# Optimization experiments

Measured on AMD Instinct MI355X. Metric: run time of the kernel, lower is better.

The kernel has to match this reference:

```python
import jax, jax.numpy as jnp
import numpy as np

B, V = 128, 128000
NEG_INF = float('-inf')


def _apply_top_k(logits, top_ks):
    vocab = logits.shape[-1]
    valid_k = jnp.where(top_ks > 0, jnp.minimum(top_ks, vocab), vocab)  # [B]
    order = jnp.argsort(-logits, axis=-1)                 # descending sort indices [B,V]
    sorted_logits = jnp.take_along_axis(logits, order, axis=-1)
    ranks = jnp.arange(vocab)[None, :]                    # [1,V]
    keep = ranks < valid_k[:, None]
    masked_sorted = jnp.where(keep, sorted_logits, NEG_INF)
    rows = jnp.arange(logits.shape[0])[:, None]
    return jnp.zeros_like(logits).at[rows, order].set(masked_sorted)


def _apply_top_p(logits, top_ps):
    order = jnp.argsort(-logits, axis=-1)
    sorted_logits = jnp.take_along_axis(logits, order, axis=-1)
    sorted_probs = jax.nn.softmax(sorted_logits, axis=-1)
    cum = jnp.cumsum(sorted_probs, axis=-1)
    keep = cum < top_ps[:, None]
    keep = keep.at[:, 0].set(True)                        # always keep the top token
    masked_sorted = jnp.where(keep, sorted_logits, NEG_INF)
    rows = jnp.arange(logits.shape[0])[:, None]
    return jnp.zeros_like(logits).at[rows, order].set(masked_sorted)


def setup_inputs() -> dict:
    key = jax.random.key(0)
    k1, k2, k3, k4, k5 = jax.random.split(key, 5)
    logits = jax.random.normal(k1, (B, V), dtype=jnp.float32) * 4.0
    temperatures = jax.random.uniform(k2, (B,), dtype=jnp.float32) + 0.5  # [0.5, 1.5)
    top_ks = jax.random.randint(k3, (B,), 0, 100, dtype=jnp.int64)        # 0 -> disabled
    top_ps = jax.random.uniform(k4, (B,), dtype=jnp.float32)
    # uniform noise; reference converts to Exp(1) via -log(u)
    exp_noise_u = jax.random.uniform(k5, (B, V), dtype=jnp.float32, minval=1e-12, maxval=1.0)
    return {"logits": logits, "temperatures": temperatures, "top_ks": top_ks,
            "top_ps": top_ps, "exp_noise_u": exp_noise_u}


def reference(logits, temperatures, top_ks, top_ps, exp_noise_u):
    x = logits.astype(jnp.float32) / temperatures[:, None]
    x = _apply_top_k(x, top_ks)
    x = _apply_top_p(x, top_ps)
    probs = jax.nn.softmax(x, axis=-1)
    q = jnp.clip(-jnp.log(exp_noise_u), 1e-10)            # Exp(1) samples, clamped like torch
    sample_tokens = jnp.argmax(probs / q, axis=-1)
    return sample_tokens
```

## Files before the change

### kernel.cpp

```cpp
#include <hip/hip_runtime.h>
#include <math.h>

#define SA 8
#define SM 64
#define NB 4096
#define TA 256
#define TAA 512
#define HS 256
#define TBB 1024
#define SCT 256
#define CH (NB / SCT)
#define CAPSEG 512
#define GTOT (SA * CAPSEG)
#define MAXM1 16
#define GB1 16384
#define SUBC 512
#define EQC 64
#define FXS 1099511627776.0f
#define FXI (1.0f / 1099511627776.0f)

typedef unsigned u32;
typedef unsigned long long u64;

struct State {
  float m, Z2;
  int mode, k, r, eqn;
  u32 vstar;
  int eq[EQC];
};

struct Aux1 {
  u32 pfx;
  int ca;
  float ea;
  float S;
  float target;
};

struct ScanSh {
  u32 axc[SCT]; float axe[SCT];
  u32 sufc[SCT]; float sufe[SCT];
  int cbin[SCT]; u32 cca[SCT]; float cea[SCT];
  int fbin[SCT]; u32 fca[SCT]; float fea[SCT];
};

__device__ __forceinline__ u32 f2key(float f) {
  u32 u = __float_as_uint(f);
  return u ^ ((u >> 31) ? 0xFFFFFFFFu : 0x80000000u);
}
__device__ __forceinline__ float key2f(u32 k) {
  u32 u = (k & 0x80000000u) ? (k ^ 0x80000000u) : ~k;
  return __uint_as_float(u);
}
__device__ __forceinline__ int is_mode0(int k, int V) {
  return (k >= 1 && k <= 256 && k < V);
}

__device__ void scan_level(const u32* cnt, const u64* e0, ScanSh* ax,
                           u32* sprefix, int* scnt_above, float* sexp_above,
                           float target, int tid) {
  if (tid < SCT) {
    u32 cc = 0; float ce = 0.f; const int base = tid * CH;
    for (int j = 0; j < CH; ++j) { cc += cnt[base + j]; ce += (float)e0[base + j] * FXI; }
    ax->axc[tid] = cc; ax->axe[tid] = ce;
  }
  __syncthreads();
  if (tid == 0) {
    u32 rc = 0; float re = 0.f;
    for (int c = SCT - 1; c >= 0; --c) {
      ax->sufc[c] = rc; ax->sufe[c] = re;
      rc += ax->axc[c]; re += ax->axe[c];
    }
  }
  __syncthreads();
  if (tid < SCT) {
    const int base = tid * CH;
    u32 rc = ax->sufc[tid]; float re = ax->sufe[tid];
    int best = -1; u32 bca = 0; float bea = 0.f;
    int fb = -1; u32 ffca = 0; float ffea = 0.f;
    for (int b = base + CH - 1; b >= base; --b) {
      u32 c = cnt[b]; float ebv = (float)e0[b] * FXI;
      bool cross = (c > 0) && ((re + ebv) >= target);
      if (cross && best < 0) { best = b; bca = rc; bea = re; }
      if (c > 0) { fb = b; ffca = rc; ffea = re; }
      rc += c; re += ebv;
    }
    ax->cbin[tid] = best; ax->cca[tid] = bca; ax->cea[tid] = bea;
    ax->fbin[tid] = fb; ax->fca[tid] = ffca; ax->fea[tid] = ffea;
  }
  __syncthreads();
  if (tid == 0) {
    int bsel = -1; u32 ca = 0; float ea = 0.f;
    for (int c = 0; c < SCT; ++c) {
      int b = ax->cbin[c];
      if (b > bsel) { bsel = b; ca = ax->cca[c]; ea = ax->cea[c]; }
    }
    if (bsel < 0) {
      for (int c = 0; c < SCT; ++c) {
        int b = ax->fbin[c];
        if (b >= 0 && (bsel < 0 || b < bsel)) { bsel = b; ca = ax->fca[c]; ea = ax->fea[c]; }
      }
    }
    if (bsel < 0) bsel = 0;
    *sprefix = (u32)bsel;
    *scnt_above = (int)ca;
    *sexp_above = ea;
  }
  __syncthreads();
}

__global__ __launch_bounds__(TAA) void kA(const float* __restrict__ logits,
                                          const float* __restrict__ temps,
                                          const int* __restrict__ topks,
                                          float* __restrict__ maxpart,
                                          u32* __restrict__ scnt,
                                          float* __restrict__ candv,
                                          int* __restrict__ candi,
                                          u32* __restrict__ nm1, int V) {
  const int row = blockIdx.x, seg = blockIdx.y, tid = threadIdx.x;
  __shared__ u32 cnt[NB];
  __shared__ float sm[TAA];
  __shared__ u32 cs[HS];
  __shared__ int bb[HS];
  __shared__ int lcnt;
  __shared__ u32 sT;
  if (row == 0 && seg == 0 && tid == 0) nm1[0] = 0;
  const int k = topks[row];
  const int m0 = is_mode0(k, V);
  const float t = temps[row];
  const float* lr = logits + (size_t)row * V;
  const float4* l4 = (const float4*)lr;
  const int n4 = V >> 2;
  const int q0 = (int)((long long)seg * n4 / SA);
  const int q1 = (int)((long long)(seg + 1) * n4 / SA);
  float mx = -INFINITY;
  if (m0) {
    for (int i = tid; i < NB; i += TAA) cnt[i] = 0;
    if (tid == 0) lcnt = 0;
    __syncthreads();
    for (int i = q0 + tid; i < q1; i += TAA) {
      float4 v = l4[i];
      float xs[4] = {v.x / t, v.y / t, v.z / t, v.w / t};
#pragma unroll
      for (int j = 0; j < 4; ++j) {
        mx = fmaxf(mx, xs[j]);
        atomicAdd(&cnt[f2key(xs[j]) >> 20], 1u);
      }
    }
    if (seg == SA - 1)
      for (int i = (n4 << 2) + tid; i < V; i += TAA) {
        float x = lr[i] / t;
        mx = fmaxf(mx, x);
        atomicAdd(&cnt[f2key(x) >> 20], 1u);
      }
  } else {
    for (int i = q0 + tid; i < q1; i += TAA) {
      float4 v = l4[i];
      mx = fmaxf(mx, fmaxf(fmaxf(v.x, v.y), fmaxf(v.z, v.w)) / t);
    }
    if (seg == SA - 1)
      for (int i = (n4 << 2) + tid; i < V; i += TAA) mx = fmaxf(mx, lr[i] / t);
  }
  sm[tid] = mx;
  __syncthreads();
  for (int s = TAA >> 1; s > 0; s >>= 1) {
    if (tid < s) sm[tid] = fmaxf(sm[tid], sm[tid + s]);
    __syncthreads();
  }
  if (tid == 0) maxpart[row * SA + seg] = sm[0];
  if (!m0) return;
  if (tid < HS) {
    u32 cc = 0; const int base = tid * (NB / HS);
    for (int j = 0; j < NB / HS; ++j) cc += cnt[base + j];
    cs[tid] = cc;
  }
  __syncthreads();
  if (tid == 0) {
    u32 rc = 0;
    for (int c = HS - 1; c >= 0; --c) { u32 tmp = cs[c]; cs[c] = rc; rc += tmp; }
  }
  __syncthreads();
  const int kk = (k > 256) ? 256 : k;
  if (tid < HS) {
    const int base = tid * (NB / HS);
    u32 rc = cs[tid]; int best = -1;
    for (int b = base + NB / HS - 1; b >= base; --b) {
      u32 c = cnt[b];
      if (c && best < 0 && (int)(rc + c) >= kk) best = b;
      rc += c;
    }
    bb[tid] = best;
  }
  __syncthreads();
  if (tid == 0) {
    int bsel = -1;
    for (int c = 0; c < HS; ++c) if (bb[c] > bsel) bsel = bb[c];
    if (bsel < 0) { for (int b = 0; b < NB; ++b) if (cnt[b]) { bsel = b; break; } }
    if (bsel < 0) bsel = 0;
    sT = ((u32)bsel) << 20;
  }
  __syncthreads();
  const u32 T = sT;
  const size_t cbase = ((size_t)row * SA + seg) * CAPSEG;
  for (int i = q0 + tid; i < q1; i += TAA) {
    float4 v = l4[i];
    float xs[4] = {v.x / t, v.y / t, v.z / t, v.w / t};
#pragma unroll
    for (int j = 0; j < 4; ++j) {
      if (f2key(xs[j]) >= T) {
        int s = atomicAdd(&lcnt, 1);
        if (s < CAPSEG) { candv[cbase + s] = xs[j]; candi[cbase + s] = i * 4 + j; }
      }
    }
  }
  if (seg == SA - 1)
    for (int i = (n4 << 2) + tid; i < V; i += TAA) {
      float x = lr[i] / t;
      if (f2key(x) >= T) {
        int s = atomicAdd(&lcnt, 1);
        if (s < CAPSEG) { candv[cbase + s] = x; candi[cbase + s] = i; }
      }
    }
  __syncthreads();
  if (tid == 0) { int n = lcnt; if (n > CAPSEG) n = CAPSEG; scnt[row * SA + seg] = (u32)n; }
}

__global__ __launch_bounds__(TBB) void kB(const int* __restrict__ topks,
                                          const float* __restrict__ maxpart,
                                          State* __restrict__ st,
                                          u64* __restrict__ rpack,
                                          u32* __restrict__ nm1,
                                          u32* __restrict__ m1rows,
                                          u32* __restrict__ zp, size_t zwords, int V) {
  const int row = blockIdx.x, tid = threadIdx.x;
  State* rs = &st[row];
  const int k = topks[row];
  const int m0 = is_mode0(k, V);
  if (tid == 0) {
    float m = maxpart[row * SA];
    for (int j = 1; j < SA; ++j) m = fmaxf(m, maxpart[row * SA + j]);
    rs->m = m; rs->mode = m0 ? 0 : 1; rs->k = k; rs->eqn = 0; rs->r = 0;
    if (!m0) {
      int idx = (int)atomicAdd(nm1, 1u);
      if (idx < MAXM1) m1rows[idx] = (u32)row;
      rpack[row] = 0ull;
    }
  }
  const size_t stride = (size_t)gridDim.x * blockDim.x;
  for (size_t i = (size_t)blockIdx.x * blockDim.x + tid; i < zwords; i += stride) zp[i] = 0;
}

__global__ __launch_bounds__(TA) void kC(const float* __restrict__ logits,
                                         const float* __restrict__ temps,
                                         const State* __restrict__ st,
                                         const u32* __restrict__ nm1,
                                         const u32* __restrict__ m1rows,
                                         float* __restrict__ Sparts,
                                         u32* __restrict__ m1c0,
                                         u64* __restrict__ m1e0, int V) {
  u32 n = nm1[0]; if (n > MAXM1) n = MAXM1;
  if (blockIdx.x >= n) return;
  const int row = (int)m1rows[blockIdx.x];
  const int m1 = blockIdx.x, seg = blockIdx.y, tid = threadIdx.x;
  const State* rs = &st[row];
  __shared__ u32 c0[NB];
  __shared__ u64 e0[NB];
  __shared__ float ss[TA];
  for (int i = tid; i < NB; i += TA) { c0[i] = 0; e0[i] = 0ull; }
  __syncthreads();
  const float t = temps[row];
  const float m = rs->m;
  const float* lr = logits + (size_t)row * V;
  const float4* l4 = (const float4*)lr;
  const int n4 = V >> 2;
  const int q0 = (int)((long long)seg * n4 / SM);
  const int q1 = (int)((long long)(seg + 1) * n4 / SM);
  float ls = 0.f;
  for (int i = q0 + tid; i < q1; i += TA) {
    float4 v = l4[i];
    float xs[4] = {v.x / t, v.y / t, v.z / t, v.w / t};
#pragma unroll
    for (int j = 0; j < 4; ++j) {
      float e = expf(xs[j] - m);
      ls += e;
      u32 b = f2key(xs[j]) >> 20;
      atomicAdd(&c0[b], 1u);
      u64 fx = (u64)(e * FXS);
      if (fx) atomicAdd(&e0[b], fx);
    }
  }
  if (seg == SM - 1)
    for (int i = (n4 << 2) + tid; i < V; i += TA) {
      float x = lr[i] / t;
      float e = expf(x - m);
      ls += e;
      u32 b = f2key(x) >> 20;
      atomicAdd(&c0[b], 1u);
      u64 fx = (u64)(e * FXS);
      if (fx) atomicAdd(&e0[b], fx);
    }
  ss[tid] = ls;
  __syncthreads();
  for (int s = TA >> 1; s > 0; s >>= 1) {
    if (tid < s) ss[tid] += ss[tid + s];
    __syncthreads();
  }
  if (tid == 0) Sparts[m1 * SM + seg] = ss[0];
  for (int b = tid; b < NB; b += TA) {
    if (c0[b]) atomicAdd(&m1c0[(size_t)m1 * NB + b], c0[b]);
    if (e0[b]) atomicAdd(&m1e0[(size_t)m1 * NB + b], e0[b]);
  }
}

__global__ __launch_bounds__(TA) void kC2(const float* __restrict__ topps,
                                          const u32* __restrict__ nm1,
                                          const u32* __restrict__ m1rows,
                                          const float* __restrict__ Sparts,
                                          const u32* __restrict__ m1c0,
                                          const u64* __restrict__ m1e0,
                                          Aux1* __restrict__ aux1) {
  u32 n = nm1[0]; if (n > MAXM1) n = MAXM1;
  if (blockIdx.x >= n) return;
  const int row = (int)m1rows[blockIdx.x];
  const int m1 = blockIdx.x, tid = threadIdx.x;
  __shared__ u32 cnt[NB];
  __shared__ u64 e0[NB];
  __shared__ ScanSh ax;
  __shared__ u32 spfx;
  __shared__ int sca;
  __shared__ float sea;
  for (int i = tid; i < NB; i += TA) {
    cnt[i] = m1c0[(size_t)m1 * NB + i];
    e0[i] = m1e0[(size_t)m1 * NB + i];
  }
  __syncthreads();
  float S = 0.f;
  for (int j = 0; j < SM; ++j) S += Sparts[m1 * SM + j];
  const float target = topps[row] * S;
  scan_level(cnt, e0, &ax, &spfx, &sca, &sea, target, tid);
  if (tid == 0) {
    Aux1 a; a.pfx = spfx; a.ca = sca; a.ea = sea; a.S = S; a.target = target;
    aux1[m1] = a;
  }
}

__global__ __launch_bounds__(TA) void kD(const float* __restrict__ logits,
                                         const float* __restrict__ temps,
                                         const u32* __restrict__ nm1,
                                         const u32* __restrict__ m1rows,
                                         const Aux1* __restrict__ aux1,
                                         u32* __restrict__ gcnt1,
                                         float* __restrict__ g1v,
                                         int* __restrict__ g1i, int V) {
  u32 n = nm1[0]; if (n > MAXM1) n = MAXM1;
  if (blockIdx.x >= n) return;
  const int row = (int)m1rows[blockIdx.x];
  const int m1 = blockIdx.x, seg = blockIdx.y, tid = threadIdx.x;
  const u32 pfx = aux1[m1].pfx;
  const float t = temps[row];
  const float* lr = logits + (size_t)row * V;
  const float4* l4 = (const float4*)lr;
  const int n4 = V >> 2;
  const int q0 = (int)((long long)seg * n4 / SM);
  const int q1 = (int)((long long)(seg + 1) * n4 / SM);
  const size_t base = (size_t)m1 * GB1;
  for (int i = q0 + tid; i < q1; i += TA) {
    float4 v = l4[i];
    float xs[4] = {v.x / t, v.y / t, v.z / t, v.w / t};
#pragma unroll
    for (int j = 0; j < 4; ++j) {
      if ((f2key(xs[j]) >> 20) == pfx) {
        u32 s = atomicAdd(&gcnt1[m1], 1u);
        if (s < GB1) { g1v[base + s] = xs[j]; g1i[base + s] = i * 4 + j; }
      }
    }
  }
  if (seg == SM - 1)
    for (int i = (n4 << 2) + tid; i < V; i += TA) {
      float x = lr[i] / t;
      if ((f2key(x) >> 20) == pfx) {
        u32 s = atomicAdd(&gcnt1[m1], 1u);
        if (s < GB1) { g1v[base + s] = x; g1i[base + s] = i; }
      }
    }
}

__global__ __launch_bounds__(TBB) void kD2(const float* __restrict__ topps,
                                           const u32* __restrict__ nm1,
                                           const u32* __restrict__ m1rows,
                                           const Aux1* __restrict__ aux1,
                                           const u32* __restrict__ gcnt1,
                                           const float* __restrict__ g1v,
                                           const int* __restrict__ g1i,
                                           State* __restrict__ st) {
  u32 n = nm1[0]; if (n > MAXM1) n = MAXM1;
  if (blockIdx.x >= n) return;
  const int row = (int)m1rows[blockIdx.x];
  const int m1 = blockIdx.x, tid = threadIdx.x;
  State* rs = &st[row];
  __shared__ u32 cnt1[1024];
  __shared__ u64 fx1[1024];
  __shared__ u32 csuf[1024];
  __shared__ u64 esuf[1024];
  __shared__ float subv[SUBC]; __shared__ int subi[SUBC];
  __shared__ float ssv[SUBC]; __shared__ int ssi[SUBC];
  __shared__ int scross, sfb, sca1, sns;
  __shared__ float sea1;
  int nf = (int)gcnt1[m1]; if (nf > GB1) nf = GB1;
  cnt1[tid] = 0; fx1[tid] = 0ull;
  if (tid == 0) { sns = 0; scross = -1; sfb = 0x7FFFFFFF; }
  __syncthreads();
  const float m = rs->m;
  const size_t base = (size_t)m1 * GB1;
  for (int i = tid; i < nf; i += TBB) {
    float x = g1v[base + i];
    u32 b = (f2key(x) >> 10) & 0x3FFu;
    float e = expf(x - m);
    atomicAdd(&cnt1[b], 1u);
    u64 fx = (u64)(e * FXS);
    if (fx) atomicAdd(&fx1[b], fx);
  }
  __syncthreads();
  csuf[tid] = cnt1[tid]; esuf[tid] = fx1[tid];
  __syncthreads();
  for (int stp = 1; stp < 1024; stp <<= 1) {
    u32 ca_ = 0; u64 ea_ = 0ull;
    if (tid + stp < 1024) { ca_ = csuf[tid + stp]; ea_ = esuf[tid + stp]; }
    __syncthreads();
    csuf[tid] += ca_; esuf[tid] += ea_;
    __syncthreads();
  }
  {
    const float ea0 = aux1[m1].ea;
    const float target = aux1[m1].target;
    u32 c = cnt1[tid];
    if (c) {
      float racc = (float)(esuf[tid] - fx1[tid]) * FXI;
      float ebv = (float)fx1[tid] * FXI;
      if (ea0 + (racc + ebv) >= target) atomicMax(&scross, tid);
      atomicMin(&sfb, tid);
    }
  }
  __syncthreads();
  if (tid == 0) {
    const float ea0 = aux1[m1].ea;
    const int ca0 = aux1[m1].ca;
    int cb = scross;
    if (cb < 0) cb = (sfb != 0x7FFFFFFF) ? sfb : 0;
    u32 cAbove = csuf[cb] - cnt1[cb];
    float eAbove = (float)(esuf[cb] - fx1[cb]) * FXI;
    scross = cb;
    sea1 = ea0 + eAbove;
    sca1 = ca0 + (int)cAbove;
  }
  __syncthreads();
  const u32 cb = (u32)scross;
  for (int i = tid; i < nf; i += TBB) {
    float x = g1v[base + i];
    if (((f2key(x) >> 10) & 0x3FFu) == cb) {
      int s = atomicAdd(&sns, 1);
      if (s < SUBC) { subv[s] = x; subi[s] = g1i[base + i]; }
    }
  }
  __syncthreads();
  int ns = sns; if (ns > SUBC) ns = SUBC;
  for (int i = tid; i < ns; i += TBB) {
    float v = subv[i]; int ix = subi[i];
    int rank = 0;
    for (int j = 0; j < ns; ++j) {
      float vj = subv[j]; int ij = subi[j];
      if (vj > v || (vj == v && ij < ix)) rank++;
    }
    ssv[rank] = v; ssi[rank] = ix;
  }
  __syncthreads();
  if (tid == 0) {
    const float S = aux1[m1].S;
    const float p = topps[row];
    float run_n = sea1 / S;
    float run_u = sea1;
    const int have_above = (sca1 > 0);
    u32 lastkey = 0u; int lastr = 0, laststart = -1, anykept = 0;
    u32 vsel = 0u; int rsel = -1, bstart = 0;
    int j = 0;
    while (j < ns) {
      u32 key = f2key(ssv[j]);
      int c = 1;
      while (j + c < ns && f2key(ssv[j + c]) == key) ++c;
      float e = expf(ssv[j] - m);
      float en = e / S;
      int kept = 0;
      for (int q = 0; q < c; ++q) {
        float nn = run_n + en;
        if (nn < p) { run_n = nn; run_u += e; kept++; } else break;
      }
      if (kept == c) { lastkey = key; lastr = c; laststart = j; anykept = 1; j += c; continue; }
      if (kept > 0) { vsel = key; rsel = kept; bstart = j; }
      else if (anykept) { vsel = lastkey; rsel = lastr; bstart = laststart; }
      else if (have_above) { vsel = key; rsel = 0; bstart = j; }
      else { vsel = key; rsel = 1; bstart = j; run_u += e; }
      break;
    }
    if (rsel < 0) {
      if (anykept) { vsel = lastkey; rsel = lastr; bstart = laststart; }
      else if (ns > 0) {
        vsel = f2key(ssv[0]); bstart = 0;
        if (have_above) rsel = 0;
        else { rsel = 1; run_u += expf(ssv[0] - m); }
      } else { vsel = 0u; rsel = 0; bstart = 0; }
    }
    int eqn = rsel;
    if (eqn > EQC) eqn = EQC;
    if (eqn < 0) eqn = 0;
    if (bstart + eqn > ns) eqn = ns - bstart;
    if (eqn < 0) eqn = 0;
    for (int q2 = 0; q2 < eqn; ++q2) rs->eq[q2] = ssi[bstart + q2];
    rs->eqn = eqn; rs->r = rsel; rs->vstar = vsel; rs->Z2 = run_u;
  }
}

__global__ __launch_bounds__(TBB) void kH(const float* __restrict__ topps,
                                          const float* __restrict__ noise,
                                          const u32* __restrict__ scnt,
                                          const float* __restrict__ candv,
                                          const int* __restrict__ candi,
                                          const State* __restrict__ st,
                                          int* __restrict__ out, int V) {
  const int row = blockIdx.x, tid = threadIdx.x;
  const State* rs = &st[row];
  if (rs->mode != 0) return;
  __shared__ float gv[GTOT]; __shared__ int gi[GTOT];
  __shared__ float sv[CAPSEG]; __shared__ int si[CAPSEG];
  __shared__ float fv[CAPSEG]; __shared__ int fi[CAPSEG];
  __shared__ float pe[CAPSEG];
  __shared__ float rr[TBB]; __shared__ int ri[TBB];
  __shared__ int offs[SA + 1];
  __shared__ u32 dh[256]; __shared__ u32 dsufx[256];
  __shared__ u32 sPrefix; __shared__ int sRemain, sNf, sDig;
  __shared__ int sJ; __shared__ float sZ2;
  if (tid == 0) {
    int o = 0;
    for (int s = 0; s < SA; ++s) {
      offs[s] = o;
      int c = (int)scnt[row * SA + s];
      if (c > CAPSEG) c = CAPSEG;
      if (c < 0) c = 0;
      o += c;
    }
    offs[SA] = o;
  }
  __syncthreads();
  const int g = offs[SA];
  for (int s = 0; s < SA; ++s) {
    const int o = offs[s], c = offs[s + 1] - o;
    const size_t cbase = ((size_t)row * SA + s) * CAPSEG;
    for (int i = tid; i < c; i += TBB) { gv[o + i] = candv[cbase + i]; gi[o + i] = candi[cbase + i]; }
  }
  __syncthreads();
  int kk = rs->k; if (kk > 256) kk = 256; if (kk > g) kk = g;
  if (tid == 0) { sPrefix = 0u; sRemain = (kk < 1) ? 1 : kk; }
  __syncthreads();
  for (int pass = 0; pass < 4; ++pass) {
    const int shift = 24 - 8 * pass;
    if (tid < 256) dh[tid] = 0;
    if (tid == 0) sDig = -1;
    __syncthreads();
    const u32 pref = sPrefix;
    for (int i = tid; i < g; i += TBB) {
      u32 key = f2key(gv[i]);
      if (pass == 0 || (key >> (shift + 8)) == pref)
        atomicAdd(&dh[(key >> shift) & 0xFFu], 1u);
    }
    __syncthreads();
    if (tid < 256) dsufx[tid] = dh[tid];
    __syncthreads();
    for (int stp = 1; stp < 256; stp <<= 1) {
      u32 addv = 0;
      if (tid < 256 && tid + stp < 256) addv = dsufx[tid + stp];
      __syncthreads();
      if (tid < 256) dsufx[tid] += addv;
      __syncthreads();
    }
    if (tid < 256) {
      u32 excl = dsufx[tid] - dh[tid];
      u32 rem = (u32)sRemain;
      if (dh[tid] && excl < rem && excl + dh[tid] >= rem) sDig = tid;
    }
    __syncthreads();
    if (tid == 0) {
      int d = sDig; if (d < 0) d = 0;
      u32 excl = dsufx[d] - dh[d];
      sRemain -= (int)excl;
      sPrefix = (sPrefix << 8) | (u32)d;
      if (pass == 3) sNf = 0;
    }
    __syncthreads();
  }
  const u32 Tk = sPrefix;
  for (int i = tid; i < g; i += TBB) {
    if (f2key(gv[i]) >= Tk) {
      int s = atomicAdd(&sNf, 1);
      if (s < CAPSEG) { fv[s] = gv[i]; fi[s] = gi[i]; }
    }
  }
  __syncthreads();
  int nf = sNf; if (nf > CAPSEG) nf = CAPSEG;
  for (int i = tid; i < nf; i += TBB) {
    float v = fv[i]; int ix = fi[i];
    int rank = 0;
    for (int j = 0; j < nf; ++j) {
      float vj = fv[j]; int ij = fi[j];
      if (vj > v || (vj == v && ij < ix)) rank++;
    }
    sv[rank] = v; si[rank] = ix;
  }
  __syncthreads();
  const float m = rs->m;
  const float p = topps[row];
  int keff = rs->k; if (keff > nf) keff = nf;
  for (int j = tid; j < keff; j += TBB) pe[j] = expf(sv[j] - m);
  __syncthreads();
  if (tid == 0) {
    int J = 1; float Z2 = 1.f;
    if (nf > 0 && keff > 0) {
      float Zk = 0.f;
      for (int j = 0; j < keff; ++j) Zk += pe[j];
      float c = 0.f; int Jc = 0;
      for (int j = 0; j < keff; ++j) {
        float pr = pe[j] / Zk;
        c += pr;
        if (c < p) Jc++;
      }
      if (Jc < 1) Jc = 1;
      J = Jc;
      Z2 = 0.f;
      for (int j = 0; j < J && j < keff; ++j) Z2 += pe[j];
    }
    sJ = J; sZ2 = Z2;
  }
  __syncthreads();
  const int J = sJ; const float Z2 = sZ2;
  float best = -1.f; int bidx = 0x7FFFFFFF;
  for (int j = tid; j < J && j < nf; j += TBB) {
    int ix = si[j];
    float u = noise[(size_t)row * V + ix];
    float q = fmaxf(-logf(u), 1e-10f);
    float pr = pe[j] / Z2;
    float rt = pr / q;
    if (rt > best || (rt == best && ix < bidx)) { best = rt; bidx = ix; }
  }
  rr[tid] = best; ri[tid] = bidx;
  __syncthreads();
  for (int s = TBB >> 1; s > 0; s >>= 1) {
    if (tid < s) {
      float ov = rr[tid + s]; int oi = ri[tid + s];
      if (ov > rr[tid] || (ov == rr[tid] && oi < ri[tid])) { rr[tid] = ov; ri[tid] = oi; }
    }
    __syncthreads();
  }
  if (tid == 0) out[row] = (nf > 0) ? ri[0] : 0;
}

__global__ __launch_bounds__(TA) void kI(const float* __restrict__ logits,
                                         const float* __restrict__ temps,
                                         const float* __restrict__ noise,
                                         const State* __restrict__ st,
                                         u64* __restrict__ rpack,
                                         u32* __restrict__ rdone,
                                         int* __restrict__ out, int V) {
  const int row = blockIdx.x, seg = blockIdx.y, tid = threadIdx.x;
  const State* rs = &st[row];
  if (rs->mode != 1) return;
  __shared__ int eqs[EQC]; __shared__ int seqn;
  __shared__ float rr[TA]; __shared__ int ri[TA];
  if (tid == 0) {
    int nn = rs->eqn; if (nn > EQC) nn = EQC; if (nn < 0) nn = 0;
    seqn = nn;
    for (int i = 0; i < nn; ++i) eqs[i] = rs->eq[i];
  }
  __syncthreads();
  const float t = temps[row];
  const float m = rs->m;
  const float Z2 = rs->Z2;
  const u32 vk = rs->vstar;
  const int eqn = seqn;
  const float* lr = logits + (size_t)row * V;
  const float* ur = noise + (size_t)row * V;
  const float4* l4 = (const float4*)lr;
  const float4* u4 = (const float4*)ur;
  const int n4 = V >> 2;
  const int q0 = (int)((long long)seg * n4 / SM);
  const int q1 = (int)((long long)(seg + 1) * n4 / SM);
  float best = -1.f; int bidx = 0x7FFFFFFF;
  for (int i = q0 + tid; i < q1; i += TA) {
    float4 xv = l4[i];
    float4 uv = u4[i];
    float xs[4] = {xv.x / t, xv.y / t, xv.z / t, xv.w / t};
    float us[4] = {uv.x, uv.y, uv.z, uv.w};
#pragma unroll
    for (int j = 0; j < 4; ++j) {
      u32 key = f2key(xs[j]);
      bool kept = key > vk;
      if (!kept && key == vk) {
        int idx = i * 4 + j;
        for (int e = 0; e < eqn; ++e) if (eqs[e] == idx) { kept = true; break; }
      }
      if (kept) {
        float pr = expf(xs[j] - m) / Z2;
        float q = fmaxf(-logf(us[j]), 1e-10f);
        float rt = pr / q;
        int idx = i * 4 + j;
        if (rt > best || (rt == best && idx < bidx)) { best = rt; bidx = idx; }
      }
    }
  }
  if (seg == SM - 1)
    for (int i = (n4 << 2) + tid; i < V; i += TA) {
      float x = lr[i] / t;
      u32 key = f2key(x);
      bool kept = key > vk;
      if (!kept && key == vk) {
        for (int e = 0; e < eqn; ++e) if (eqs[e] == i) { kept = true; break; }
      }
      if (kept) {
        float pr = expf(x - m) / Z2;
        float q = fmaxf(-logf(ur[i]), 1e-10f);
        float rt = pr / q;
        if (rt > best || (rt == best && i < bidx)) { best = rt; bidx = i; }
      }
    }
  rr[tid] = best; ri[tid] = bidx;
  __syncthreads();
  for (int s = TA >> 1; s > 0; s >>= 1) {
    if (tid < s) {
      float ov = rr[tid + s]; int oi = ri[tid + s];
      if (ov > rr[tid] || (ov == rr[tid] && oi < ri[tid])) { rr[tid] = ov; ri[tid] = oi; }
    }
    __syncthreads();
  }
  if (tid == 0) {
    if (rr[0] >= 0.f) {
      u64 pk = ((u64)f2key(rr[0]) << 32) | (u64)(0xFFFFFFFFu - (u32)ri[0]);
      atomicMax(&rpack[row], pk);
    }
    __threadfence();
    u32 arr = atomicAdd(&rdone[row], 1u);
    if (arr == (u32)(SM - 1)) {
      u64 v = atomicAdd(&rpack[row], 0ull);
      out[row] = (int)(0xFFFFFFFFu - (u32)(v & 0xFFFFFFFFull));
    }
  }
}

extern "C" void kernel_launch(void* const* d_in, const int* in_sizes, int n_in,
                              void* d_out, int out_size, void* d_ws, size_t ws_size,
                              hipStream_t stream) {
  const float* logits = (const float*)d_in[0];
  const float* temps = (const float*)d_in[1];
  const int* topks = (const int*)d_in[2];
  const float* topps = (const float*)d_in[3];
  const float* noise = (const float*)d_in[4];
  int* out = (int*)d_out;
  const int B = in_sizes[1];
  const int V = in_sizes[0] / B;
  (void)n_in; (void)out_size; (void)ws_size;

  u32* w = (u32*)d_ws;
  size_t o = 0;
  float* maxpart = (float*)(w + o); o += (size_t)B * SA;
  u32* scnt = w + o; o += (size_t)B * SA;
  float* candv = (float*)(w + o); o += (size_t)B * SA * CAPSEG;
  int* candi = (int*)(w + o); o += (size_t)B * SA * CAPSEG;
  if (o & 1) o += 1;
  u64* rpack = (u64*)(w + o); o += 2 * (size_t)B;
  u32* nm1 = w + o; o += 1;
  u32* m1rows = w + o; o += MAXM1;
  if (o & 1) o += 1;
  const size_t zbase = o;
  u64* m1e0 = (u64*)(w + o); o += 2 * (size_t)MAXM1 * NB;
  u32* m1c0 = w + o; o += (size_t)MAXM1 * NB;
  u32* gcnt1 = w + o; o += MAXM1;
  u32* rdone = w + o; o += (size_t)B;
  const size_t zwords = o - zbase;
  float* Sparts = (float*)(w + o); o += (size_t)MAXM1 * SM;
  Aux1* aux1 = (Aux1*)(w + o); o += (sizeof(Aux1) / 4) * (size_t)MAXM1;
  float* g1v = (float*)(w + o); o += (size_t)MAXM1 * GB1;
  int* g1i = (int*)(w + o); o += (size_t)MAXM1 * GB1;
  State* st = (State*)(w + o);

  kA<<<dim3(B, SA), TAA, 0, stream>>>(logits, temps, topks, maxpart, scnt, candv, candi, nm1, V);
  kB<<<B, TBB, 0, stream>>>(topks, maxpart, st, rpack, nm1, m1rows, w + zbase, zwords, V);
  kC<<<dim3(MAXM1, SM), TA, 0, stream>>>(logits, temps, st, nm1, m1rows, Sparts, m1c0, m1e0, V);
  kC2<<<MAXM1, TA, 0, stream>>>(topps, nm1, m1rows, Sparts, m1c0, m1e0, aux1);
  kD<<<dim3(MAXM1, SM), TA, 0, stream>>>(logits, temps, nm1, m1rows, aux1, gcnt1, g1v, g1i, V);
  kD2<<<MAXM1, TBB, 0, stream>>>(topps, nm1, m1rows, aux1, gcnt1, g1v, g1i, st);
  kH<<<B, TBB, 0, stream>>>(topps, noise, scnt, candv, candi, st, out, V);
  kI<<<dim3(B, SM), TA, 0, stream>>>(logits, temps, noise, st, rpack, rdone, out, V);
}
```

Before: 247.3 us.

## Fuse mode-1 top-p pipeline into one per-row kernel, drop state buffers

Merges the separate mode-1 stages (histogram, scan, gather, refine, final sampling) into a single kernel with one 1024-thread block per row, so intermediates stay in shared memory. This removes the zeroing kernel, the global State/aux buffers and the cross-block atomic reduction, cutting eight launches to three. In exchange, each mode-1 row is handled by one block that streams the whole vocabulary several times, so per-row parallelism drops from 64 segments to one block. The slot for each row is found by a serial count over earlier rows.

New measurement: 295.2 us. 1.19x slower.

```diff
diff --git a/kernel.cpp b/kernel.cpp
--- a/kernel.cpp
+++ b/kernel.cpp
@@ -2,9 +2,7 @@
 #include <math.h>
 
 #define SA 8
-#define SM 64
 #define NB 4096
-#define TA 256
 #define TAA 512
 #define HS 256
 #define TBB 1024
@@ -22,21 +20,6 @@
 typedef unsigned u32;
 typedef unsigned long long u64;
 
-struct State {
-  float m, Z2;
-  int mode, k, r, eqn;
-  u32 vstar;
-  int eq[EQC];
-};
-
-struct Aux1 {
-  u32 pfx;
-  int ca;
-  float ea;
-  float S;
-  float target;
-};
-
 struct ScanSh {
   u32 axc[SCT]; float axe[SCT];
   u32 sufc[SCT]; float sufe[SCT];
@@ -47,10 +30,6 @@
 __device__ __forceinline__ u32 f2key(float f) {
   u32 u = __float_as_uint(f);
   return u ^ ((u >> 31) ? 0xFFFFFFFFu : 0x80000000u);
-}
-__device__ __forceinline__ float key2f(u32 k) {
-  u32 u = (k & 0x80000000u) ? (k ^ 0x80000000u) : ~k;
-  return __uint_as_float(u);
 }
 __device__ __forceinline__ int is_mode0(int k, int V) {
   return (k >= 1 && k <= 256 && k < V);
@@ -115,8 +94,7 @@
                                           float* __restrict__ maxpart,
                                           u32* __restrict__ scnt,
                                           float* __restrict__ candv,
-                                          int* __restrict__ candi,
-                                          u32* __restrict__ nm1, int V) {
+                                          int* __restrict__ candi, int V) {
   const int row = blockIdx.x, seg = blockIdx.y, tid = threadIdx.x;
   __shared__ u32 cnt[NB];
   __shared__ float sm[TAA];
@@ -124,7 +102,6 @@
   __shared__ int bb[HS];
   __shared__ int lcnt;
   __shared__ u32 sT;
-  if (row == 0 && seg == 0 && tid == 0) nm1[0] = 0;
   const int k = topks[row];
   const int m0 = is_mode0(k, V);
   const float t = temps[row];
@@ -225,58 +202,203 @@
   if (tid == 0) { int n = lcnt; if (n > CAPSEG) n = CAPSEG; scnt[row * SA + seg] = (u32)n; }
 }
 
-__global__ __launch_bounds__(TBB) void kB(const int* __restrict__ topks,
+__global__ __launch_bounds__(TBB) void kH(const float* __restrict__ topps,
+                                          const float* __restrict__ noise,
+                                          const int* __restrict__ topks,
                                           const float* __restrict__ maxpart,
-                                          State* __restrict__ st,
-                                          u64* __restrict__ rpack,
-                                          u32* __restrict__ nm1,
-                                          u32* __restrict__ m1rows,
-                                          u32* __restrict__ zp, size_t zwords, int V) {
+                                          const u32* __restrict__ scnt,
+                                          const float* __restrict__ candv,
+                                          const int* __restrict__ candi,
+                                          int* __restrict__ out, int V) {
   const int row = blockIdx.x, tid = threadIdx.x;
-  State* rs = &st[row];
+  const int kR = topks[row];
+  if (!is_mode0(kR, V)) return;
+  __shared__ float gv[GTOT]; __shared__ int gi[GTOT];
+  __shared__ float sv[CAPSEG]; __shared__ int si[CAPSEG];
+  __shared__ float fv[CAPSEG]; __shared__ int fi[CAPSEG];
+  __shared__ float pe[CAPSEG];
+  __shared__ float rr[TBB]; __shared__ int ri[TBB];
+  __shared__ int offs[SA + 1];
+  __shared__ u32 dh[256]; __shared__ u32 dsufx[256];
+  __shared__ u32 sPrefix; __shared__ int sRemain, sNf, sDig;
+  __shared__ int sJ; __shared__ float sZ2;
+  if (tid == 0) {
+    int o = 0;
+    for (int s = 0; s < SA; ++s) {
+      offs[s] = o;
+      int c = (int)scnt[row * SA + s];
+      if (c > CAPSEG) c = CAPSEG;
+      if (c < 0) c = 0;
+      o += c;
+    }
+    offs[SA] = o;
+  }
+  __syncthreads();
+  const int g = offs[SA];
+  for (int s = 0; s < SA; ++s) {
+    const int o = offs[s], c = offs[s + 1] - o;
+    const size_t cbase = ((size_t)row * SA + s) * CAPSEG;
+    for (int i = tid; i < c; i += TBB) { gv[o + i] = candv[cbase + i]; gi[o + i] = candi[cbase + i]; }
+  }
+  __syncthreads();
+  int kk = kR; if (kk > 256) kk = 256; if (kk > g) kk = g;
+  if (tid == 0) { sPrefix = 0u; sRemain = (kk < 1) ? 1 : kk; }
+  __syncthreads();
+  for (int pass = 0; pass < 4; ++pass) {
+    const int shift = 24 - 8 * pass;
+    if (tid < 256) dh[tid] = 0;
+    if (tid == 0) sDig = -1;
+    __syncthreads();
+    const u32 pref = sPrefix;
+    for (int i = tid; i < g; i += TBB) {
+      u32 key = f2key(gv[i]);
+      if (pass == 0 || (key >> (shift + 8)) == pref)
+        atomicAdd(&dh[(key >> shift) & 0xFFu], 1u);
+    }
+    __syncthreads();
+    if (tid < 256) dsufx[tid] = dh[tid];
+    __syncthreads();
+    for (int stp = 1; stp < 256; stp <<= 1) {
+      u32 addv = 0;
+      if (tid < 256 && tid + stp < 256) addv = dsufx[tid + stp];
+      __syncthreads();
+      if (tid < 256) dsufx[tid] += addv;
+      __syncthreads();
+    }
+    if (tid < 256) {
+      u32 excl = dsufx[tid] - dh[tid];
+      u32 rem = (u32)sRemain;
+      if (dh[tid] && excl < rem && excl + dh[tid] >= rem) sDig = tid;
+    }
+    __syncthreads();
+    if (tid == 0) {
+      int d = sDig; if (d < 0) d = 0;
+      u32 excl = dsufx[d] - dh[d];
+      sRemain -= (int)excl;
+      sPrefix = (sPrefix << 8) | (u32)d;
+      if (pass == 3) sNf = 0;
+    }
+    __syncthreads();
+  }
+  const u32 Tk = sPrefix;
+  for (int i = tid; i < g; i += TBB) {
+    if (f2key(gv[i]) >= Tk) {
+      int s = atomicAdd(&sNf, 1);
+      if (s < CAPSEG) { fv[s] = gv[i]; fi[s] = gi[i]; }
+    }
+  }
+  __syncthreads();
+  int nf = sNf; if (nf > CAPSEG) nf = CAPSEG;
+  for (int i = tid; i < nf; i += TBB) {
+    float v = fv[i]; int ix = fi[i];
+    int rank = 0;
+    for (int j = 0; j < nf; ++j) {
+      float vj = fv[j]; int ij = fi[j];
+      if (vj > v || (vj == v && ij < ix)) rank++;
+    }
+    sv[rank] = v; si[rank] = ix;
+  }
+  __syncthreads();
+  float m;
+  { float mm = maxpart[row * SA];
+    for (int j = 1; j < SA; ++j) mm = fmaxf(mm, maxpart[row * SA + j]);
+    m = mm; }
+  const float p = topps[row];
+  int keff = kR; if (keff > nf) keff = nf;
+  for (int j = tid; j < keff; j += TBB) pe[j] = expf(sv[j] - m);
+  __syncthreads();
+  if (tid == 0) {
+    int J = 1; float Z2 = 1.f;
+    if (nf > 0 && keff > 0) {
+      float Zk = 0.f;
+      for (int j = 0; j < keff; ++j) Zk += pe[j];
+      float c = 0.f; int Jc = 0;
+      for (int j = 0; j < keff; ++j) {
+        float pr = pe[j] / Zk;
+        c += pr;
+        if (c < p) Jc++;
+      }
+      if (Jc < 1) Jc = 1;
+      J = Jc;
+      Z2 = 0.f;
+      for (int j = 0; j < J && j < keff; ++j) Z2 += pe[j];
+    }
+    sJ = J; sZ2 = Z2;
+  }
+  __syncthreads();
+  const int J = sJ; const float Z2 = sZ2;
+  float best = -1.f; int bidx = 0x7FFFFFFF;
+  for (int j = tid; j < J && j < nf; j += TBB) {
+    int ix = si[j];
+    float u = noise[(size_t)row * V + ix];
+    float q = fmaxf(-logf(u), 1e-10f);
+    float pr = pe[j] / Z2;
+    float rt = pr / q;
+    if (rt > best || (rt == best && ix < bidx)) { best = rt; bidx = ix; }
+  }
+  rr[tid] = best; ri[tid] = bidx;
+  __syncthreads();
+  for (int s = TBB >> 1; s > 0; s >>= 1) {
+    if (tid < s) {
+      float ov = rr[tid + s]; int oi = ri[tid + s];
+      if (ov > rr[tid] || (ov == rr[tid] && oi < ri[tid])) { rr[tid] = ov; ri[tid] = oi; }
+    }
+    __syncthreads();
+  }
+  if (tid == 0) out[row] = (nf > 0) ? ri[0] : 0;
+}
+
+__global__ __launch_bounds__(TBB) void kM1(const float* __restrict__ logits,
+                                           const float* __restrict__ temps,
+                                           const int* __restrict__ topks,
+                                           const float* __restrict__ topps,
+                                           const float* __restrict__ noise,
+                                           const float* __restrict__ maxpart,
+                                           float* __restrict__ g1v,
+                                           int* __restrict__ g1i,
+                                           int* __restrict__ out, int V) {
+  const int row = blockIdx.x, tid = threadIdx.x;
   const int k = topks[row];
-  const int m0 = is_mode0(k, V);
-  if (tid == 0) {
-    float m = maxpart[row * SA];
-    for (int j = 1; j < SA; ++j) m = fmaxf(m, maxpart[row * SA + j]);
-    rs->m = m; rs->mode = m0 ? 0 : 1; rs->k = k; rs->eqn = 0; rs->r = 0;
-    if (!m0) {
-      int idx = (int)atomicAdd(nm1, 1u);
-      if (idx < MAXM1) m1rows[idx] = (u32)row;
-      rpack[row] = 0ull;
-    }
-  }
-  const size_t stride = (size_t)gridDim.x * blockDim.x;
-  for (size_t i = (size_t)blockIdx.x * blockDim.x + tid; i < zwords; i += stride) zp[i] = 0;
-}
-
-__global__ __launch_bounds__(TA) void kC(const float* __restrict__ logits,
-                                         const float* __restrict__ temps,
-                                         const State* __restrict__ st,
-                                         const u32* __restrict__ nm1,
-                                         const u32* __restrict__ m1rows,
-                                         float* __restrict__ Sparts,
-                                         u32* __restrict__ m1c0,
-                                         u64* __restrict__ m1e0, int V) {
-  u32 n = nm1[0]; if (n > MAXM1) n = MAXM1;
-  if (blockIdx.x >= n) return;
-  const int row = (int)m1rows[blockIdx.x];
-  const int m1 = blockIdx.x, seg = blockIdx.y, tid = threadIdx.x;
-  const State* rs = &st[row];
-  __shared__ u32 c0[NB];
+  if (is_mode0(k, V)) return;
+  __shared__ int sslot;
+  if (tid == 0) {
+    int c = 0;
+    for (int r = 0; r < row; ++r) if (!is_mode0(topks[r], V)) ++c;
+    sslot = c;
+  }
+  __syncthreads();
+  const int slot = sslot;
+  if (slot >= MAXM1) return;
+
+  __shared__ u32 cnt[NB];
   __shared__ u64 e0[NB];
-  __shared__ float ss[TA];
-  for (int i = tid; i < NB; i += TA) { c0[i] = 0; e0[i] = 0ull; }
-  __syncthreads();
+  __shared__ ScanSh ax;
+  __shared__ float ss[TBB];
+  __shared__ u32 cnt1[1024]; __shared__ u64 fx1[1024];
+  __shared__ u32 csuf[1024]; __shared__ u64 esuf[1024];
+  __shared__ float subv[SUBC]; __shared__ int subi[SUBC];
+  __shared__ float ssv[SUBC]; __shared__ int ssi[SUBC];
+  __shared__ float rr[TBB]; __shared__ int ri[TBB];
+  __shared__ int eqs[EQC];
+  __shared__ u32 spfx; __shared__ int sca; __shared__ float sea;
+  __shared__ int sgc, scross, sfb, sca1, sns, seqn;
+  __shared__ float sea1, sZ2; __shared__ u32 svstar;
+
+  for (int i = tid; i < NB; i += TBB) { cnt[i] = 0; e0[i] = 0ull; }
+  if (tid == 0) { sgc = 0; sns = 0; scross = -1; sfb = 0x7FFFFFFF; }
+  __syncthreads();
+
   const float t = temps[row];
-  const float m = rs->m;
+  float m;
+  { float mm = maxpart[row * SA];
+    for (int j = 1; j < SA; ++j) mm = fmaxf(mm, maxpart[row * SA + j]);
+    m = mm; }
   const float* lr = logits + (size_t)row * V;
   const float4* l4 = (const float4*)lr;
   const int n4 = V >> 2;
-  const int q0 = (int)((long long)seg * n4 / SM);
-  const int q1 = (int)((long long)(seg + 1) * n4 / SM);
+
   float ls = 0.f;
-  for (int i = q0 + tid; i < q1; i += TA) {
+  for (int i = tid; i < n4; i += TBB) {
     float4 v = l4[i];
     float xs[4] = {v.x / t, v.y / t, v.z / t, v.w / t};
 #pragma unroll
@@ -284,136 +406,58 @@
       float e = expf(xs[j] - m);
       ls += e;
       u32 b = f2key(xs[j]) >> 20;
-      atomicAdd(&c0[b], 1u);
+      atomicAdd(&cnt[b], 1u);
       u64 fx = (u64)(e * FXS);
       if (fx) atomicAdd(&e0[b], fx);
     }
   }
-  if (seg == SM - 1)
-    for (int i = (n4 << 2) + tid; i < V; i += TA) {
-      float x = lr[i] / t;
-      float e = expf(x - m);
-      ls += e;
-      u32 b = f2key(x) >> 20;
-      atomicAdd(&c0[b], 1u);
-      u64 fx = (u64)(e * FXS);
-      if (fx) atomicAdd(&e0[b], fx);
-    }
+  for (int i = (n4 << 2) + tid; i < V; i += TBB) {
+    float x = lr[i] / t;
+    float e = expf(x - m);
+    ls += e;
+    u32 b = f2key(x) >> 20;
+    atomicAdd(&cnt[b], 1u);
+    u64 fx = (u64)(e * FXS);
+    if (fx) atomicAdd(&e0[b], fx);
+  }
   ss[tid] = ls;
   __syncthreads();
-  for (int s = TA >> 1; s > 0; s >>= 1) {
+  for (int s = TBB >> 1; s > 0; s >>= 1) {
     if (tid < s) ss[tid] += ss[tid + s];
     __syncthreads();
   }
-  if (tid == 0) Sparts[m1 * SM + seg] = ss[0];
-  for (int b = tid; b < NB; b += TA) {
-    if (c0[b]) atomicAdd(&m1c0[(size_t)m1 * NB + b], c0[b]);
-    if (e0[b]) atomicAdd(&m1e0[(size_t)m1 * NB + b], e0[b]);
-  }
-}
-
-__global__ __launch_bounds__(TA) void kC2(const float* __restrict__ topps,
-                                          const u32* __restrict__ nm1,
-                                          const u32* __restrict__ m1rows,
-                                          const float* __restrict__ Sparts,
-                                          const u32* __restrict__ m1c0,
-                                          const u64* __restrict__ m1e0,
-                                          Aux1* __restrict__ aux1) {
-  u32 n = nm1[0]; if (n > MAXM1) n = MAXM1;
-  if (blockIdx.x >= n) return;
-  const int row = (int)m1rows[blockIdx.x];
-  const int m1 = blockIdx.x, tid = threadIdx.x;
-  __shared__ u32 cnt[NB];
-  __shared__ u64 e0[NB];
-  __shared__ ScanSh ax;
-  __shared__ u32 spfx;
-  __shared__ int sca;
-  __shared__ float sea;
-  for (int i = tid; i < NB; i += TA) {
-    cnt[i] = m1c0[(size_t)m1 * NB + i];
-    e0[i] = m1e0[(size_t)m1 * NB + i];
-  }
-  __syncthreads();
-  float S = 0.f;
-  for (int j = 0; j < SM; ++j) S += Sparts[m1 * SM + j];
+  const float S = ss[0];
   const float target = topps[row] * S;
+
   scan_level(cnt, e0, &ax, &spfx, &sca, &sea, target, tid);
-  if (tid == 0) {
-    Aux1 a; a.pfx = spfx; a.ca = sca; a.ea = sea; a.S = S; a.target = target;
-    aux1[m1] = a;
-  }
-}
-
-__global__ __launch_bounds__(TA) void kD(const float* __restrict__ logits,
-                                         const float* __restrict__ temps,
-                                         const u32* __restrict__ nm1,
-                                         const u32* __restrict__ m1rows,
-                                         const Aux1* __restrict__ aux1,
-                                         u32* __restrict__ gcnt1,
-                                         float* __restrict__ g1v,
-                                         int* __restrict__ g1i, int V) {
-  u32 n = nm1[0]; if (n > MAXM1) n = MAXM1;
-  if (blockIdx.x >= n) return;
-  const int row = (int)m1rows[blockIdx.x];
-  const int m1 = blockIdx.x, seg = blockIdx.y, tid = threadIdx.x;
-  const u32 pfx = aux1[m1].pfx;
-  const float t = temps[row];
-  const float* lr = logits + (size_t)row * V;
-  const float4* l4 = (const float4*)lr;
-  const int n4 = V >> 2;
-  const int q0 = (int)((long long)seg * n4 / SM);
-  const int q1 = (int)((long long)(seg + 1) * n4 / SM);
-  const size_t base = (size_t)m1 * GB1;
-  for (int i = q0 + tid; i < q1; i += TA) {
+  const u32 pfx = spfx;
+
+  const size_t gbase = (size_t)slot * GB1;
+  for (int i = tid; i < n4; i += TBB) {
     float4 v = l4[i];
     float xs[4] = {v.x / t, v.y / t, v.z / t, v.w / t};
 #pragma unroll
     for (int j = 0; j < 4; ++j) {
       if ((f2key(xs[j]) >> 20) == pfx) {
-        u32 s = atomicAdd(&gcnt1[m1], 1u);
-        if (s < GB1) { g1v[base + s] = xs[j]; g1i[base + s] = i * 4 + j; }
-      }
-    }
-  }
-  if (seg == SM - 1)
-    for (int i = (n4 << 2) + tid; i < V; i += TA) {
-      float x = lr[i] / t;
-      if ((f2key(x) >> 20) == pfx) {
-        u32 s = atomicAdd(&gcnt1[m1], 1u);
-        if (s < GB1) { g1v[base + s] = x; g1i[base + s] = i; }
-      }
-    }
-}
-
-__global__ __launch_bounds__(TBB) void kD2(const float* __restrict__ topps,
-                                           const u32* __restrict__ nm1,
-                                           const u32* __restrict__ m1rows,
-                                           const Aux1* __restrict__ aux1,
-                                           const u32* __restrict__ gcnt1,
-                                           const float* __restrict__ g1v,
-                                           const int* __restrict__ g1i,
-                                           State* __restrict__ st) {
-  u32 n = nm1[0]; if (n > MAXM1) n = MAXM1;
-  if (blockIdx.x >= n) return;
-  const int row = (int)m1rows[blockIdx.x];
-  const int m1 = blockIdx.x, tid = threadIdx.x;
-  State* rs = &st[row];
-  __shared__ u32 cnt1[1024];
-  __shared__ u64 fx1[1024];
-  __shared__ u32 csuf[1024];
-  __shared__ u64 esuf[1024];
-  __shared__ float subv[SUBC]; __shared__ int subi[SUBC];
-  __shared__ float ssv[SUBC]; __shared__ int ssi[SUBC];
-  __shared__ int scross, sfb, sca1, sns;
-  __shared__ float sea1;
-  int nf = (int)gcnt1[m1]; if (nf > GB1) nf = GB1;
+        int s2 = atomicAdd(&sgc, 1);
+        if (s2 < GB1) { g1v[gbase + s2] = xs[j]; g1i[gbase + s2] = i * 4 + j; }
+      }
+    }
+  }
+  for (int i = (n4 << 2) + tid; i < V; i += TBB) {
+    float x = lr[i] / t;
+    if ((f2key(x) >> 20) == pfx) {
+      int s2 = atomicAdd(&sgc, 1);
+      if (s2 < GB1) { g1v[gbase + s2] = x; g1i[gbase + s2] = i; }
+    }
+  }
+  __syncthreads();
+  int nf = sgc; if (nf > GB1) nf = GB1;
+
   cnt1[tid] = 0; fx1[tid] = 0ull;
-  if (tid == 0) { sns = 0; scross = -1; sfb = 0x7FFFFFFF; }
-  __syncthreads();
-  const float m = rs->m;
-  const size_t base = (size_t)m1 * GB1;
+  __syncthreads();
   for (int i = tid; i < nf; i += TBB) {
-    float x = g1v[base + i];
+    float x = g1v[gbase + i];
     u32 b = (f2key(x) >> 10) & 0x3FFu;
     float e = expf(x - m);
     atomicAdd(&cnt1[b], 1u);
@@ -431,35 +475,32 @@
     __syncthreads();
   }
   {
-    const float ea0 = aux1[m1].ea;
-    const float target = aux1[m1].target;
     u32 c = cnt1[tid];
     if (c) {
       float racc = (float)(esuf[tid] - fx1[tid]) * FXI;
       float ebv = (float)fx1[tid] * FXI;
-      if (ea0 + (racc + ebv) >= target) atomicMax(&scross, tid);
+      if (sea + (racc + ebv) >= target) atomicMax(&scross, tid);
       atomicMin(&sfb, tid);
     }
   }
   __syncthreads();
   if (tid == 0) {
-    const float ea0 = aux1[m1].ea;
-    const int ca0 = aux1[m1].ca;
     int cb = scross;
     if (cb < 0) cb = (sfb != 0x7FFFFFFF) ? sfb : 0;
     u32 cAbove = csuf[cb] - cnt1[cb];
     float eAbove = (float)(esuf[cb] - fx1[cb]) * FXI;
     scross = cb;
-    sea1 = ea0 + eAbove;
-    sca1 = ca0 + (int)cAbove;
+    sea1 = sea + eAbove;
+    sca1 = sca + (int)cAbove;
   }
   __syncthreads();
   const u32 cb = (u32)scross;
+
   for (int i = tid; i < nf; i += TBB) {
-    float x = g1v[base + i];
+    float x = g1v[gbase + i];
     if (((f2key(x) >> 10) & 0x3FFu) == cb) {
-      int s = atomicAdd(&sns, 1);
-      if (s < SUBC) { subv[s] = x; subi[s] = g1i[base + i]; }
+      int s2 = atomicAdd(&sns, 1);
+      if (s2 < SUBC) { subv[s2] = x; subi[s2] = g1i[gbase + i]; }
     }
   }
   __syncthreads();
@@ -467,15 +508,14 @@
   for (int i = tid; i < ns; i += TBB) {
     float v = subv[i]; int ix = subi[i];
     int rank = 0;
-    for (int j = 0; j < ns; ++j) {
-      float vj = subv[j]; int ij = subi[j];
+    for (int j2 = 0; j2 < ns; ++j2) {
+      float vj = subv[j2]; int ij = subi[j2];
       if (vj > v || (vj == v && ij < ix)) rank++;
     }
     ssv[rank] = v; ssi[rank] = ix;
   }
   __syncthreads();
   if (tid == 0) {
-    const float S = aux1[m1].S;
     const float p = topps[row];
     float run_n = sea1 / S;
     float run_u = sea1;
@@ -514,185 +554,18 @@
     if (eqn < 0) eqn = 0;
     if (bstart + eqn > ns) eqn = ns - bstart;
     if (eqn < 0) eqn = 0;
-    for (int q2 = 0; q2 < eqn; ++q2) rs->eq[q2] = ssi[bstart + q2];
-    rs->eqn = eqn; rs->r = rsel; rs->vstar = vsel; rs->Z2 = run_u;
-  }
-}
-
-__global__ __launch_bounds__(TBB) void kH(const float* __restrict__ topps,
-                                          const float* __restrict__ noise,
-                                          const u32* __restrict__ scnt,
-                                          const float* __restrict__ candv,
-                                          const int* __restrict__ candi,
-                                          const State* __restrict__ st,
-                                          int* __restrict__ out, int V) {
-  const int row = blockIdx.x, tid = threadIdx.x;
-  const State* rs = &st[row];
-  if (rs->mode != 0) return;
-  __shared__ float gv[GTOT]; __shared__ int gi[GTOT];
-  __shared__ float sv[CAPSEG]; __shared__ int si[CAPSEG];
-  __shared__ float fv[CAPSEG]; __shared__ int fi[CAPSEG];
-  __shared__ float pe[CAPSEG];
-  __shared__ float rr[TBB]; __shared__ int ri[TBB];
-  __shared__ int offs[SA + 1];
-  __shared__ u32 dh[256]; __shared__ u32 dsufx[256];
-  __shared__ u32 sPrefix; __shared__ int sRemain, sNf, sDig;
-  __shared__ int sJ; __shared__ float sZ2;
-  if (tid == 0) {
-    int o = 0;
-    for (int s = 0; s < SA; ++s) {
-      offs[s] = o;
-      int c = (int)scnt[row * SA + s];
-      if (c > CAPSEG) c = CAPSEG;
-      if (c < 0) c = 0;
-      o += c;
-    }
-    offs[SA] = o;
-  }
-  __syncthreads();
-  const int g = offs[SA];
-  for (int s = 0; s < SA; ++s) {
-    const int o = offs[s], c = offs[s + 1] - o;
-    const size_t cbase = ((size_t)row * SA + s) * CAPSEG;
-    for (int i = tid; i < c; i += TBB) { gv[o + i] = candv[cbase + i]; gi[o + i] = candi[cbase + i]; }
-  }
-  __syncthreads();
-  int kk = rs->k; if (kk > 256) kk = 256; if (kk > g) kk = g;
-  if (tid == 0) { sPrefix = 0u; sRemain = (kk < 1) ? 1 : kk; }
-  __syncthreads();
-  for (int pass = 0; pass < 4; ++pass) {
-    const int shift = 24 - 8 * pass;
-    if (tid < 256) dh[tid] = 0;
-    if (tid == 0) sDig = -1;
-    __syncthreads();
-    const u32 pref = sPrefix;
-    for (int i = tid; i < g; i += TBB) {
-      u32 key = f2key(gv[i]);
-      if (pass == 0 || (key >> (shift + 8)) == pref)
-        atomicAdd(&dh[(key >> shift) & 0xFFu], 1u);
-    }
-    __syncthreads();
-    if (tid < 256) dsufx[tid] = dh[tid];
-    __syncthreads();
-    for (int stp = 1; stp < 256; stp <<= 1) {
-      u32 addv = 0;
-      if (tid < 256 && tid + stp < 256) addv = dsufx[tid + stp];
-      __syncthreads();
-      if (tid < 256) dsufx[tid] += addv;
-      __syncthreads();
-    }
-    if (tid < 256) {
-      u32 excl = dsufx[tid] - dh[tid];
-      u32 rem = (u32)sRemain;
-      if (dh[tid] && excl < rem && excl + dh[tid] >= rem) sDig = tid;
-    }
-    __syncthreads();
-    if (tid == 0) {
-      int d = sDig; if (d < 0) d = 0;
-      u32 excl = dsufx[d] - dh[d];
-      sRemain -= (int)excl;
-      sPrefix = (sPrefix << 8) | (u32)d;
-      if (pass == 3) sNf = 0;
-    }
-    __syncthreads();
-  }
-  const u32 Tk = sPrefix;
-  for (int i = tid; i < g; i += TBB) {
-    if (f2key(gv[i]) >= Tk) {
-      int s = atomicAdd(&sNf, 1);
-      if (s < CAPSEG) { fv[s] = gv[i]; fi[s] = gi[i]; }
-    }
-  }
-  __syncthreads();
-  int nf = sNf; if (nf > CAPSEG) nf = CAPSEG;
-  for (int i = tid; i < nf; i += TBB) {
-    float v = fv[i]; int ix = fi[i];
-    int rank = 0;
-    for (int j = 0; j < nf; ++j) {
-      float vj = fv[j]; int ij = fi[j];
-      if (vj > v || (vj == v && ij < ix)) rank++;
-    }
-    sv[rank] = v; si[rank] = ix;
-  }
-  __syncthreads();
-  const float m = rs->m;
-  const float p = topps[row];
-  int keff = rs->k; if (keff > nf) keff = nf;
-  for (int j = tid; j < keff; j += TBB) pe[j] = expf(sv[j] - m);
-  __syncthreads();
-  if (tid == 0) {
-    int J = 1; float Z2 = 1.f;
-    if (nf > 0 && keff > 0) {
-      float Zk = 0.f;
-      for (int j = 0; j < keff; ++j) Zk += pe[j];
-      float c = 0.f; int Jc = 0;
-      for (int j = 0; j < keff; ++j) {
-        float pr = pe[j] / Zk;
-        c += pr;
-        if (c < p) Jc++;
-      }
-      if (Jc < 1) Jc = 1;
-      J = Jc;
-      Z2 = 0.f;
-      for (int j = 0; j < J && j < keff; ++j) Z2 += pe[j];
-    }
-    sJ = J; sZ2 = Z2;
-  }
-  __syncthreads();
-  const int J = sJ; const float Z2 = sZ2;
+    for (int q2 = 0; q2 < eqn; ++q2) eqs[q2] = ssi[bstart + q2];
+    seqn = eqn; svstar = vsel; sZ2 = run_u;
+  }
+  __syncthreads();
+
+  const float Z2 = sZ2;
+  const u32 vk = svstar;
+  const int eqn = seqn;
+  const float* ur = noise + (size_t)row * V;
+  const float4* u4 = (const float4*)ur;
   float best = -1.f; int bidx = 0x7FFFFFFF;
-  for (int j = tid; j < J && j < nf; j += TBB) {
-    int ix = si[j];
-    float u = noise[(size_t)row * V + ix];
-    float q = fmaxf(-logf(u), 1e-10f);
-    float pr = pe[j] / Z2;
-    float rt = pr / q;
-    if (rt > best || (rt == best && ix < bidx)) { best = rt; bidx = ix; }
-  }
-  rr[tid] = best; ri[tid] = bidx;
-  __syncthreads();
-  for (int s = TBB >> 1; s > 0; s >>= 1) {
-    if (tid < s) {
-      float ov = rr[tid + s]; int oi = ri[tid + s];
-      if (ov > rr[tid] || (ov == rr[tid] && oi < ri[tid])) { rr[tid] = ov; ri[tid] = oi; }
-    }
-    __syncthreads();
-  }
-  if (tid == 0) out[row] = (nf > 0) ? ri[0] : 0;
-}
-
-__global__ __launch_bounds__(TA) void kI(const float* __restrict__ logits,
-                                         const float* __restrict__ temps,
-                                         const float* __restrict__ noise,
-                                         const State* __restrict__ st,
-                                         u64* __restrict__ rpack,
-                                         u32* __restrict__ rdone,
-                                         int* __restrict__ out, int V) {
-  const int row = blockIdx.x, seg = blockIdx.y, tid = threadIdx.x;
-  const State* rs = &st[row];
-  if (rs->mode != 1) return;
-  __shared__ int eqs[EQC]; __shared__ int seqn;
-  __shared__ float rr[TA]; __shared__ int ri[TA];
-  if (tid == 0) {
-    int nn = rs->eqn; if (nn > EQC) nn = EQC; if (nn < 0) nn = 0;
-    seqn = nn;
-    for (int i = 0; i < nn; ++i) eqs[i] = rs->eq[i];
-  }
-  __syncthreads();
-  const float t = temps[row];
-  const float m = rs->m;
-  const float Z2 = rs->Z2;
-  const u32 vk = rs->vstar;
-  const int eqn = seqn;
-  const float* lr = logits + (size_t)row * V;
-  const float* ur = noise + (size_t)row * V;
-  const float4* l4 = (const float4*)lr;
-  const float4* u4 = (const float4*)ur;
-  const int n4 = V >> 2;
-  const int q0 = (int)((long long)seg * n4 / SM);
-  const int q1 = (int)((long long)(seg + 1) * n4 / SM);
-  float best = -1.f; int bidx = 0x7FFFFFFF;
-  for (int i = q0 + tid; i < q1; i += TA) {
+  for (int i = tid; i < n4; i += TBB) {
     float4 xv = l4[i];
     float4 uv = u4[i];
     float xs[4] = {xv.x / t, xv.y / t, xv.z / t, xv.w / t};
@@ -714,42 +587,30 @@
       }
     }
   }
-  if (seg == SM - 1)
-    for (int i = (n4 << 2) + tid; i < V; i += TA) {
-      float x = lr[i] / t;
-      u32 key = f2key(x);
-      bool kept = key > vk;
-      if (!kept && key == vk) {
-        for (int e = 0; e < eqn; ++e) if (eqs[e] == i) { kept = true; break; }
-      }
-      if (kept) {
-        float pr = expf(x - m) / Z2;
-        float q = fmaxf(-logf(ur[i]), 1e-10f);
-        float rt = pr / q;
-        if (rt > best || (rt == best && i < bidx)) { best = rt; bidx = i; }
-      }
-    }
+  for (int i = (n4 << 2) + tid; i < V; i += TBB) {
+    float x = lr[i] / t;
+    u32 key = f2key(x);
+    bool kept = key > vk;
+    if (!kept && key == vk) {
+      for (int e = 0; e < eqn; ++e) if (eqs[e] == i) { kept = true; break; }
+    }
+    if (kept) {
+      float pr = expf(x - m) / Z2;
+      float q = fmaxf(-logf(ur[i]), 1e-10f);
+      float rt = pr / q;
+      if (rt > best || (rt == best && i < bidx)) { best = rt; bidx = i; }
+    }
+  }
   rr[tid] = best; ri[tid] = bidx;
   __syncthreads();
-  for (int s = TA >> 1; s > 0; s >>= 1) {
+  for (int s = TBB >> 1; s > 0; s >>= 1) {
     if (tid < s) {
       float ov = rr[tid + s]; int oi = ri[tid + s];
       if (ov > rr[tid] || (ov == rr[tid] && oi < ri[tid])) { rr[tid] = ov; ri[tid] = oi; }
     }
     __syncthreads();
   }
-  if (tid == 0) {
-    if (rr[0] >= 0.f) {
-      u64 pk = ((u64)f2key(rr[0]) << 32) | (u64)(0xFFFFFFFFu - (u32)ri[0]);
-      atomicMax(&rpack[row], pk);
-    }
-    __threadfence();
-    u32 arr = atomicAdd(&rdone[row], 1u);
-    if (arr == (u32)(SM - 1)) {
-      u64 v = atomicAdd(&rpack[row], 0ull);
-      out[row] = (int)(0xFFFFFFFFu - (u32)(v & 0xFFFFFFFFull));
-    }
-  }
+  if (tid == 0) out[row] = (rr[0] >= 0.f) ? ri[0] : 0;
 }
 
 extern "C" void kernel_launch(void* const* d_in, const int* in_sizes, int n_in,
@@ -771,29 +632,10 @@
   u32* scnt = w + o; o += (size_t)B * SA;
   float* candv = (float*)(w + o); o += (size_t)B * SA * CAPSEG;
   int* candi = (int*)(w + o); o += (size_t)B * SA * CAPSEG;
-  if (o & 1) o += 1;
-  u64* rpack = (u64*)(w + o); o += 2 * (size_t)B;
-  u32* nm1 = w + o; o += 1;
-  u32* m1rows = w + o; o += MAXM1;
-  if (o & 1) o += 1;
-  const size_t zbase = o;
-  u64* m1e0 = (u64*)(w + o); o += 2 * (size_t)MAXM1 * NB;
-  u32* m1c0 = w + o; o += (size_t)MAXM1 * NB;
-  u32* gcnt1 = w + o; o += MAXM1;
-  u32* rdone = w + o; o += (size_t)B;
-  const size_t zwords = o - zbase;
-  float* Sparts = (float*)(w + o); o += (size_t)MAXM1 * SM;
-  Aux1* aux1 = (Aux1*)(w + o); o += (sizeof(Aux1) / 4) * (size_t)MAXM1;
   float* g1v = (float*)(w + o); o += (size_t)MAXM1 * GB1;
   int* g1i = (int*)(w + o); o += (size_t)MAXM1 * GB1;
-  State* st = (State*)(w + o);
-
-  kA<<<dim3(B, SA), TAA, 0, stream>>>(logits, temps, topks, maxpart, scnt, candv, candi, nm1, V);
-  kB<<<B, TBB, 0, stream>>>(topks, maxpart, st, rpack, nm1, m1rows, w + zbase, zwords, V);
-  kC<<<dim3(MAXM1, SM), TA, 0, stream>>>(logits, temps, st, nm1, m1rows, Sparts, m1c0, m1e0, V);
-  kC2<<<MAXM1, TA, 0, stream>>>(topps, nm1, m1rows, Sparts, m1c0, m1e0, aux1);
-  kD<<<dim3(MAXM1, SM), TA, 0, stream>>>(logits, temps, nm1, m1rows, aux1, gcnt1, g1v, g1i, V);
-  kD2<<<MAXM1, TBB, 0, stream>>>(topps, nm1, m1rows, aux1, gcnt1, g1v, g1i, st);
-  kH<<<B, TBB, 0, stream>>>(topps, noise, scnt, candv, candi, st, out, V);
-  kI<<<dim3(B, SM), TA, 0, stream>>>(logits, temps, noise, st, rpack, rdone, out, V);
+
+  kA<<<dim3(B, SA), TAA, 0, stream>>>(logits, temps, topks, maxpart, scnt, candv, candi, V);
+  kH<<<B, TBB, 0, stream>>>(topps, noise, topks, maxpart, scnt, candv, candi, out, V);
+  kM1<<<B, TBB, 0, stream>>>(logits, temps, topks, topps, noise, maxpart, g1v, g1i, out, V);
 }
```
